# Performance work log

Measured on AMD Instinct MI355X. Metric: run time of the kernel, lower is better.

## Reference

```python
import jax, jax.numpy as jnp
import numpy as np

D_MODEL = 2048
D_INNER = 4096  # d_model * expand_factor
LN_EPS = 1e-5


def setup_inputs() -> dict:
    key = jax.random.key(0)
    k1, k2, k3, k4 = jax.random.split(key, 4)
    B, S = 2, 4096
    x = jax.random.normal(k1, (B, S, D_MODEL), dtype=jnp.float32)
    gamma = jnp.ones((D_MODEL,), dtype=jnp.float32)
    beta = jnp.zeros((D_MODEL,), dtype=jnp.float32)
    # nn.Linear-like small init to keep activations in-range
    W_in = jax.random.normal(k2, (2 * D_INNER, D_MODEL), dtype=jnp.float32) * 0.02
    W_out = jax.random.normal(k3, (D_MODEL, D_INNER), dtype=jnp.float32) * 0.02
    dt_min, dt_max = 0.001, 0.1
    dt = jax.random.uniform(k4, (D_INNER,), dtype=jnp.float32) * (dt_max - dt_min) + dt_min
    return {"x": x, "gamma": gamma, "beta": beta, "W_in": W_in, "W_out": W_out, "dt": dt}


def reference(x, gamma, beta, W_in, W_out, dt):
    # x: [B, S, D_MODEL]
    identity = x
    # LayerNorm over last dim
    mu = jnp.mean(x, axis=-1, keepdims=True)
    var = jnp.mean(jnp.square(x - mu), axis=-1, keepdims=True)
    xn = (x - mu) * jax.lax.rsqrt(var + LN_EPS) * gamma + beta
    # in_proj: [B, S, 2*D_INNER]
    projected = jnp.einsum("bsd,ed->bse", xn, W_in)
    z, gate = jnp.split(projected, 2, axis=-1)
    # z gated by sigmoid of clamped z (clamp only inside sigmoid)
    z_gated = z * jax.nn.sigmoid(jnp.clip(z, -15.0, 15.0))
    # temporal weighting by softmax(-dt) over d_inner
    dt_weights = jax.nn.softmax(-dt)  # [D_INNER]
    z_temporal = z_gated * dt_weights  # broadcast over [B, S, D_INNER]
    # gate path: silu on clamped gate
    output = z_temporal * jax.nn.silu(jnp.clip(gate, -15.0, 15.0))
    # out_proj back to d_model
    output = jnp.einsum("bse,de->bsd", output, W_out)
    return output + identity
```

## Files before the change

### kernel.cpp

```cpp
#include <hip/hip_runtime.h>
#include <cstdint>
#include <cstddef>

#define T_TOK 8192
#define DM    2048
#define DI    4096
#define TWO_DI 8192

typedef __attribute__((ext_vector_type(8))) short bf16x8;
typedef __attribute__((ext_vector_type(4))) float f32x4;

__device__ __forceinline__ unsigned short f2bf(float f) {
  union { float f; unsigned u; } c; c.f = f;
  unsigned u = c.u;
  unsigned r = (u + 0x7fffu + ((u >> 16) & 1u)) >> 16;
  return (unsigned short)r;
}
__device__ __forceinline__ float bf2f(unsigned short b) {
  union { unsigned u; float f; } c; c.u = ((unsigned)b) << 16;
  return c.f;
}

__global__ __launch_bounds__(256) void ln_kernel(
    const float* __restrict__ x, const float* __restrict__ gamma,
    const float* __restrict__ beta, unsigned short* __restrict__ xn) {
  const int t = blockIdx.x;
  const int tid = threadIdx.x;
  const float* row = x + (size_t)t * DM;
  float4 v0 = reinterpret_cast<const float4*>(row)[tid];
  float4 v1 = reinterpret_cast<const float4*>(row)[tid + 256];
  float s  = v0.x + v0.y + v0.z + v0.w + v1.x + v1.y + v1.z + v1.w;
  float ss = v0.x*v0.x + v0.y*v0.y + v0.z*v0.z + v0.w*v0.w
           + v1.x*v1.x + v1.y*v1.y + v1.z*v1.z + v1.w*v1.w;
  #pragma unroll
  for (int off = 32; off > 0; off >>= 1) {
    s  += __shfl_down(s, off);
    ss += __shfl_down(ss, off);
  }
  __shared__ float red[8];
  __shared__ float mu_s, inv_s;
  if ((tid & 63) == 0) { red[tid >> 6] = s; red[4 + (tid >> 6)] = ss; }
  __syncthreads();
  if (tid == 0) {
    float S  = red[0] + red[1] + red[2] + red[3];
    float SS = red[4] + red[5] + red[6] + red[7];
    float mu  = S * (1.0f / DM);
    float var = SS * (1.0f / DM) - mu * mu;
    mu_s = mu;
    inv_s = rsqrtf(var + 1e-5f);
  }
  __syncthreads();
  const float mu = mu_s, inv = inv_s;
  float4 g0 = reinterpret_cast<const float4*>(gamma)[tid];
  float4 b0 = reinterpret_cast<const float4*>(beta)[tid];
  float4 g1 = reinterpret_cast<const float4*>(gamma)[tid + 256];
  float4 b1 = reinterpret_cast<const float4*>(beta)[tid + 256];
  ushort4 o0, o1;
  o0.x = f2bf((v0.x - mu) * inv * g0.x + b0.x);
  o0.y = f2bf((v0.y - mu) * inv * g0.y + b0.y);
  o0.z = f2bf((v0.z - mu) * inv * g0.z + b0.z);
  o0.w = f2bf((v0.w - mu) * inv * g0.w + b0.w);
  o1.x = f2bf((v1.x - mu) * inv * g1.x + b1.x);
  o1.y = f2bf((v1.y - mu) * inv * g1.y + b1.y);
  o1.z = f2bf((v1.z - mu) * inv * g1.z + b1.z);
  o1.w = f2bf((v1.w - mu) * inv * g1.w + b1.w);
  reinterpret_cast<ushort4*>(xn + (size_t)t * DM)[tid]       = o0;
  reinterpret_cast<ushort4*>(xn + (size_t)t * DM)[tid + 256] = o1;
}

__global__ __launch_bounds__(256) void cvt_bf16(
    const float* __restrict__ in, unsigned short* __restrict__ out, int n4) {
  int i = blockIdx.x * 256 + threadIdx.x;
  if (i >= n4) return;
  float4 v = reinterpret_cast<const float4*>(in)[i];
  ushort4 o;
  o.x = f2bf(v.x); o.y = f2bf(v.y); o.z = f2bf(v.z); o.w = f2bf(v.w);
  reinterpret_cast<ushort4*>(out)[i] = o;
}

__global__ __launch_bounds__(256) void dt_softmax(
    const float* __restrict__ dt, float* __restrict__ w) {
  const int tid = threadIdx.x;
  float e[16];
  float local = 0.f;
  #pragma unroll
  for (int i = 0; i < 16; ++i) {
    float v = __expf(-dt[i * 256 + tid]);
    e[i] = v;
    local += v;
  }
  #pragma unroll
  for (int off = 32; off > 0; off >>= 1) local += __shfl_down(local, off);
  __shared__ float red[4];
  __shared__ float tot;
  if ((tid & 63) == 0) red[tid >> 6] = local;
  __syncthreads();
  if (tid == 0) tot = red[0] + red[1] + red[2] + red[3];
  __syncthreads();
  const float inv = 1.f / tot;
  #pragma unroll
  for (int i = 0; i < 16; ++i) w[i * 256 + tid] = e[i] * inv;
}

__device__ __forceinline__ float actf(float z, float g, float w) {
  float zc = fminf(fmaxf(z, -15.f), 15.f);
  float sz = 1.f / (1.f + __expf(-zc));
  float gc = fminf(fmaxf(g, -15.f), 15.f);
  float sg = 1.f / (1.f + __expf(-gc));
  return z * sz * w * gc * sg;
}

__global__ __launch_bounds__(256) void act_kernel(
    const unsigned short* __restrict__ proj, const float* __restrict__ dtw,
    unsigned short* __restrict__ act) {
  const long i = (long)blockIdx.x * 256 + threadIdx.x;
  const int  e4 = (int)(i & 1023);
  const long t  = i >> 10;
  const ushort4 z4 = *reinterpret_cast<const ushort4*>(proj + (t << 13) + (e4 << 2));
  const ushort4 g4 = *reinterpret_cast<const ushort4*>(proj + (t << 13) + DI + (e4 << 2));
  const float4  w4 = reinterpret_cast<const float4*>(dtw)[e4];
  ushort4 o;
  o.x = f2bf(actf(bf2f(z4.x), bf2f(g4.x), w4.x));
  o.y = f2bf(actf(bf2f(z4.y), bf2f(g4.y), w4.y));
  o.z = f2bf(actf(bf2f(z4.z), bf2f(g4.z), w4.z));
  o.w = f2bf(actf(bf2f(z4.w), bf2f(g4.w), w4.w));
  reinterpret_cast<ushort4*>(act)[i] = o;
}

#define BM 128
#define BN 128
#define BK 64

template <int EPI>
__global__ __launch_bounds__(256, 2) void gemm_nt(
    const unsigned short* __restrict__ A, const unsigned short* __restrict__ Bm,
    unsigned short* __restrict__ Cbf, float* __restrict__ Cf,
    const float* __restrict__ ident, int M, int N, int K) {
  __shared__ unsigned short lA[BM * BK];
  __shared__ unsigned short lB[BN * BK];
  const int tid  = threadIdx.x;
  const int lane = tid & 63;
  const int wave = tid >> 6;
  const int wm = (wave >> 1) << 6;
  const int wn = (wave & 1) << 6;
  const int tM = blockIdx.y * BM;
  const int tN = blockIdx.x * BN;

  f32x4 acc[4][4];
  #pragma unroll
  for (int i = 0; i < 4; ++i)
    #pragma unroll
    for (int j = 0; j < 4; ++j) acc[i][j] = f32x4{0.f, 0.f, 0.f, 0.f};

  const unsigned short* Ab = A + (size_t)tM * K;
  const unsigned short* Bb = Bm + (size_t)tN * K;

  for (int k0 = 0; k0 < K; k0 += BK) {
    #pragma unroll
    for (int i = 0; i < 4; ++i) {
      const int t8  = i * 256 + tid;
      const int row = t8 >> 3;
      const int s8  = t8 & 7;
      const int col = ((s8 ^ (row & 7)) << 3);
      __builtin_amdgcn_global_load_lds(
          (const __attribute__((address_space(1))) void*)(Ab + (size_t)row * K + k0 + col),
          (__attribute__((address_space(3))) void*)(&lA[t8 << 3]), 16, 0, 0);
      __builtin_amdgcn_global_load_lds(
          (const __attribute__((address_space(1))) void*)(Bb + (size_t)row * K + k0 + col),
          (__attribute__((address_space(3))) void*)(&lB[t8 << 3]), 16, 0, 0);
    }
    __syncthreads();

    #pragma unroll
    for (int kk = 0; kk < BK; kk += 32) {
      const int r0 = lane & 15;
      const int s8 = (((kk >> 3) + (lane >> 4)) ^ (r0 & 7)) << 3;
      bf16x8 af[4], bfr[4];
      #pragma unroll
      for (int i = 0; i < 4; ++i)
        af[i] = *reinterpret_cast<const bf16x8*>(&lA[(wm + i * 16 + r0) * BK + s8]);
      #pragma unroll
      for (int j = 0; j < 4; ++j)
        bfr[j] = *reinterpret_cast<const bf16x8*>(&lB[(wn + j * 16 + r0) * BK + s8]);
      #pragma unroll
      for (int i = 0; i < 4; ++i)
        #pragma unroll
        for (int j = 0; j < 4; ++j)
          acc[i][j] = __builtin_amdgcn_mfma_f32_16x16x32_bf16(af[i], bfr[j], acc[i][j], 0, 0, 0);
    }
    __syncthreads();
  }

  const int cn = tN + wn + (lane & 15);
  const int rm = tM + wm + ((lane >> 4) << 2);
  #pragma unroll
  for (int i = 0; i < 4; ++i) {
    #pragma unroll
    for (int r = 0; r < 4; ++r) {
      const size_t rowoff = (size_t)(rm + i * 16 + r) * N;
      #pragma unroll
      for (int j = 0; j < 4; ++j) {
        const size_t idx = rowoff + cn + j * 16;
        const float v = acc[i][j][r];
        if (EPI == 0) {
          Cbf[idx] = f2bf(v);
        } else {
          Cf[idx] = v + ident[idx];
        }
      }
    }
  }
}

extern "C" void kernel_launch(void* const* d_in, const int* in_sizes, int n_in,
                              void* d_out, int out_size, void* d_ws, size_t ws_size,
                              hipStream_t stream) {
  const float* x     = (const float*)d_in[0];
  const float* gamma = (const float*)d_in[1];
  const float* beta  = (const float*)d_in[2];
  const float* W_in  = (const float*)d_in[3];
  const float* W_out = (const float*)d_in[4];
  const float* dt    = (const float*)d_in[5];
  float* out = (float*)d_out;

  char* ws = (char*)d_ws;
  unsigned short* xn     = (unsigned short*)(ws);
  unsigned short* win_b  = (unsigned short*)(ws + ((size_t)32 << 20));
  unsigned short* wout_b = (unsigned short*)(ws + ((size_t)64 << 20));
  float*          dtw    = (float*)(ws + ((size_t)80 << 20));
  unsigned short* proj   = (unsigned short*)(ws + ((size_t)81 << 20));
  unsigned short* act    = (unsigned short*)(ws);

  ln_kernel<<<T_TOK, 256, 0, stream>>>(x, gamma, beta, xn);
  cvt_bf16<<<(TWO_DI * DM / 4 + 255) / 256, 256, 0, stream>>>(W_in, win_b, TWO_DI * DM / 4);
  cvt_bf16<<<(DM * DI / 4 + 255) / 256, 256, 0, stream>>>(W_out, wout_b, DM * DI / 4);
  dt_softmax<<<1, 256, 0, stream>>>(dt, dtw);

  gemm_nt<0><<<dim3(TWO_DI / BN, T_TOK / BM), 256, 0, stream>>>(
      xn, win_b, proj, nullptr, nullptr, T_TOK, TWO_DI, DM);

  act_kernel<<<T_TOK * DI / 4 / 256, 256, 0, stream>>>(proj, dtw, act);

  gemm_nt<1><<<dim3(DM / BN, T_TOK / BM), 256, 0, stream>>>(
      act, wout_b, nullptr, out, x, T_TOK, DM, DI);
}
```

Baseline: 604.5 us.

## Fuse gating activation into first GEMM via paired z/gate tiles

The first projection GEMM now computes matching z and gate column tiles in one 512-thread block, with half the waves on each, and applies the sigmoid/silu/dt-weight activation in the epilogue. The gate accumulators pass to the z waves through LDS in two halves. This drops the bf16 proj intermediate (a write and re-read of T×8192) and the separate activation kernel launch. In exchange LDS use and thread count per block rise, which may lower occupancy, and the epilogue is serialised across several barriers.

```diff
diff --git a/kernel.cpp b/kernel.cpp
--- a/kernel.cpp
+++ b/kernel.cpp
@@ -110,32 +110,146 @@
   return z * sz * w * gc * sg;
 }
 
-__global__ __launch_bounds__(256) void act_kernel(
-    const unsigned short* __restrict__ proj, const float* __restrict__ dtw,
-    unsigned short* __restrict__ act) {
-  const long i = (long)blockIdx.x * 256 + threadIdx.x;
-  const int  e4 = (int)(i & 1023);
-  const long t  = i >> 10;
-  const ushort4 z4 = *reinterpret_cast<const ushort4*>(proj + (t << 13) + (e4 << 2));
-  const ushort4 g4 = *reinterpret_cast<const ushort4*>(proj + (t << 13) + DI + (e4 << 2));
-  const float4  w4 = reinterpret_cast<const float4*>(dtw)[e4];
-  ushort4 o;
-  o.x = f2bf(actf(bf2f(z4.x), bf2f(g4.x), w4.x));
-  o.y = f2bf(actf(bf2f(z4.y), bf2f(g4.y), w4.y));
-  o.z = f2bf(actf(bf2f(z4.z), bf2f(g4.z), w4.z));
-  o.w = f2bf(actf(bf2f(z4.w), bf2f(g4.w), w4.w));
-  reinterpret_cast<ushort4*>(act)[i] = o;
-}
-
 #define BM 128
 #define BN 128
 #define BK 64
 
-template <int EPI>
-__global__ __launch_bounds__(256, 2) void gemm_nt(
+__global__ __launch_bounds__(512, 2) void gemm1_fused(
+    const unsigned short* __restrict__ A, const unsigned short* __restrict__ W,
+    const float* __restrict__ dtw, unsigned short* __restrict__ act) {
+  __shared__ unsigned short lds[3 * BM * BK];
+  unsigned short* lA  = lds;
+  unsigned short* lB1 = lds + BM * BK;
+  unsigned short* lB2 = lds + 2 * BM * BK;
+  float* Xbuf = reinterpret_cast<float*>(lds);
+
+  const int tid  = threadIdx.x;
+  const int lane = tid & 63;
+  const int wave = tid >> 6;
+  const int wq   = wave & 3;
+  const int wm   = (wq >> 1) << 6;
+  const int wn   = (wq & 1) << 6;
+  const bool isZ = wave < 4;
+  const int tM = blockIdx.y * BM;
+  const int tN = blockIdx.x * BN;
+
+  f32x4 acc[4][4];
+  #pragma unroll
+  for (int i = 0; i < 4; ++i)
+    #pragma unroll
+    for (int j = 0; j < 4; ++j) acc[i][j] = f32x4{0.f, 0.f, 0.f, 0.f};
+
+  const unsigned short* Ab = A + (size_t)tM * DM;
+  const unsigned short* B1 = W + (size_t)tN * DM;
+  const unsigned short* B2 = W + (size_t)(tN + DI) * DM;
+  const unsigned short* lB = isZ ? lB1 : lB2;
+
+  for (int k0 = 0; k0 < DM; k0 += BK) {
+    #pragma unroll
+    for (int i = 0; i < 2; ++i) {
+      const int t8  = i * 512 + tid;
+      const int row = t8 >> 3;
+      const int s8  = t8 & 7;
+      const int col = ((s8 ^ (row & 7)) << 3);
+      __builtin_amdgcn_global_load_lds(
+          (const __attribute__((address_space(1))) void*)(Ab + (size_t)row * DM + k0 + col),
+          (__attribute__((address_space(3))) void*)(&lA[t8 << 3]), 16, 0, 0);
+      __builtin_amdgcn_global_load_lds(
+          (const __attribute__((address_space(1))) void*)(B1 + (size_t)row * DM + k0 + col),
+          (__attribute__((address_space(3))) void*)(&lB1[t8 << 3]), 16, 0, 0);
+      __builtin_amdgcn_global_load_lds(
+          (const __attribute__((address_space(1))) void*)(B2 + (size_t)row * DM + k0 + col),
+          (__attribute__((address_space(3))) void*)(&lB2[t8 << 3]), 16, 0, 0);
+    }
+    __syncthreads();
+
+    #pragma unroll
+    for (int kk = 0; kk < BK; kk += 32) {
+      const int r0 = lane & 15;
+      const int s8 = (((kk >> 3) + (lane >> 4)) ^ (r0 & 7)) << 3;
+      bf16x8 af[4], bfr[4];
+      #pragma unroll
+      for (int i = 0; i < 4; ++i)
+        af[i] = *reinterpret_cast<const bf16x8*>(&lA[(wm + i * 16 + r0) * BK + s8]);
+      #pragma unroll
+      for (int j = 0; j < 4; ++j)
+        bfr[j] = *reinterpret_cast<const bf16x8*>(&lB[(wn + j * 16 + r0) * BK + s8]);
+      #pragma unroll
+      for (int i = 0; i < 4; ++i)
+        #pragma unroll
+        for (int j = 0; j < 4; ++j)
+          acc[i][j] = __builtin_amdgcn_mfma_f32_16x16x32_bf16(af[i], bfr[j], acc[i][j], 0, 0, 0);
+    }
+    __syncthreads();
+  }
+
+  const int c15 = lane & 15;
+  const int qr  = (lane >> 4) << 2;
+
+  if (wave == 4 || wave == 5) {
+    #pragma unroll
+    for (int i = 0; i < 4; ++i)
+      #pragma unroll
+      for (int r = 0; r < 4; ++r) {
+        const int lr = i * 16 + qr + r;
+        #pragma unroll
+        for (int j = 0; j < 4; ++j)
+          Xbuf[lr * 132 + wn + j * 16 + c15] = acc[i][j][r];
+      }
+  }
+  __syncthreads();
+  if (wave == 0 || wave == 1) {
+    float w4[4];
+    #pragma unroll
+    for (int j = 0; j < 4; ++j) w4[j] = dtw[tN + wn + j * 16 + c15];
+    #pragma unroll
+    for (int i = 0; i < 4; ++i)
+      #pragma unroll
+      for (int r = 0; r < 4; ++r) {
+        const int lr = i * 16 + qr + r;
+        const size_t rowoff = (size_t)(tM + lr) * DI + tN + wn + c15;
+        #pragma unroll
+        for (int j = 0; j < 4; ++j) {
+          const float g = Xbuf[lr * 132 + wn + j * 16 + c15];
+          act[rowoff + j * 16] = f2bf(actf(acc[i][j][r], g, w4[j]));
+        }
+      }
+  }
+  __syncthreads();
+  if (wave == 6 || wave == 7) {
+    #pragma unroll
+    for (int i = 0; i < 4; ++i)
+      #pragma unroll
+      for (int r = 0; r < 4; ++r) {
+        const int lr = i * 16 + qr + r;
+        #pragma unroll
+        for (int j = 0; j < 4; ++j)
+          Xbuf[lr * 132 + wn + j * 16 + c15] = acc[i][j][r];
+      }
+  }
+  __syncthreads();
+  if (wave == 2 || wave == 3) {
+    float w4[4];
+    #pragma unroll
+    for (int j = 0; j < 4; ++j) w4[j] = dtw[tN + wn + j * 16 + c15];
+    #pragma unroll
+    for (int i = 0; i < 4; ++i)
+      #pragma unroll
+      for (int r = 0; r < 4; ++r) {
+        const int lr = i * 16 + qr + r;
+        const size_t rowoff = (size_t)(tM + 64 + lr) * DI + tN + wn + c15;
+        #pragma unroll
+        for (int j = 0; j < 4; ++j) {
+          const float g = Xbuf[lr * 132 + wn + j * 16 + c15];
+          act[rowoff + j * 16] = f2bf(actf(acc[i][j][r], g, w4[j]));
+        }
+      }
+  }
+}
+
+__global__ __launch_bounds__(256, 2) void gemm_nt_res(
     const unsigned short* __restrict__ A, const unsigned short* __restrict__ Bm,
-    unsigned short* __restrict__ Cbf, float* __restrict__ Cf,
-    const float* __restrict__ ident, int M, int N, int K) {
+    float* __restrict__ Cf, const float* __restrict__ ident, int M, int N, int K) {
   __shared__ unsigned short lA[BM * BK];
   __shared__ unsigned short lB[BN * BK];
   const int tid  = threadIdx.x;
@@ -201,12 +315,7 @@
       #pragma unroll
       for (int j = 0; j < 4; ++j) {
         const size_t idx = rowoff + cn + j * 16;
-        const float v = acc[i][j][r];
-        if (EPI == 0) {
-          Cbf[idx] = f2bf(v);
-        } else {
-          Cf[idx] = v + ident[idx];
-        }
+        Cf[idx] = acc[i][j][r] + ident[idx];
       }
     }
   }
@@ -228,19 +337,15 @@
   unsigned short* win_b  = (unsigned short*)(ws + ((size_t)32 << 20));
   unsigned short* wout_b = (unsigned short*)(ws + ((size_t)64 << 20));
   float*          dtw    = (float*)(ws + ((size_t)80 << 20));
-  unsigned short* proj   = (unsigned short*)(ws + ((size_t)81 << 20));
-  unsigned short* act    = (unsigned short*)(ws);
+  unsigned short* act    = (unsigned short*)(ws + ((size_t)96 << 20));
 
   ln_kernel<<<T_TOK, 256, 0, stream>>>(x, gamma, beta, xn);
   cvt_bf16<<<(TWO_DI * DM / 4 + 255) / 256, 256, 0, stream>>>(W_in, win_b, TWO_DI * DM / 4);
   cvt_bf16<<<(DM * DI / 4 + 255) / 256, 256, 0, stream>>>(W_out, wout_b, DM * DI / 4);
   dt_softmax<<<1, 256, 0, stream>>>(dt, dtw);
 
-  gemm_nt<0><<<dim3(TWO_DI / BN, T_TOK / BM), 256, 0, stream>>>(
-      xn, win_b, proj, nullptr, nullptr, T_TOK, TWO_DI, DM);
-
-  act_kernel<<<T_TOK * DI / 4 / 256, 256, 0, stream>>>(proj, dtw, act);
-
-  gemm_nt<1><<<dim3(DM / BN, T_TOK / BM), 256, 0, stream>>>(
-      act, wout_b, nullptr, out, x, T_TOK, DM, DI);
-}
+  gemm1_fused<<<dim3(DI / BN, T_TOK / BM), 512, 0, stream>>>(xn, win_b, dtw, act);
+
+  gemm_nt_res<<<dim3(DM / BN, T_TOK / BM), 256, 0, stream>>>(
+      act, wout_b, out, x, T_TOK, DM, DI);
+}
```

Result: no change. 602.6 us (-0.3%).
